# Kernel tuning notes

Measured on AMD Instinct MI355X. Metric: run time of the kernel, lower is better.

Reference implementation:

```python
import jax, jax.numpy as jnp
import numpy as np

D_MODEL = 1024
NUM_HEADS = 16
D_IN = 1024

def setup_inputs() -> dict:
    key = jax.random.key(0)
    ks = jax.random.split(key, 5)
    scale = 1.0 / np.sqrt(D_IN)
    return {
        "in_features": jax.random.normal(ks[0], (4, 2048, D_IN), dtype=jnp.float32),
        "q_weight": jax.random.normal(ks[1], (D_MODEL, D_IN), dtype=jnp.float32) * scale,
        "k_weight": jax.random.normal(ks[2], (D_MODEL, D_IN), dtype=jnp.float32) * scale,
        "v_weight": jax.random.normal(ks[3], (D_MODEL, D_IN), dtype=jnp.float32) * scale,
        "o_weight": jax.random.normal(ks[4], (D_MODEL, D_MODEL), dtype=jnp.float32) * scale,
    }

def reference(in_features, q_weight, k_weight, v_weight, o_weight):
    batch, seq_len, _ = in_features.shape
    d_head = D_MODEL // NUM_HEADS
    # QKV projections (Linear with no bias: x @ W^T)
    q = jnp.einsum('bsi,di->bsd', in_features, q_weight)
    k = jnp.einsum('bsi,di->bsd', in_features, k_weight)
    v = jnp.einsum('bsi,di->bsd', in_features, v_weight)
    # split heads -> [b, h, s, d_head]
    q = q.reshape(batch, seq_len, NUM_HEADS, d_head).transpose(0, 2, 1, 3)
    k = k.reshape(batch, seq_len, NUM_HEADS, d_head).transpose(0, 2, 1, 3)
    v = v.reshape(batch, seq_len, NUM_HEADS, d_head).transpose(0, 2, 1, 3)
    # scaled dot-product attention (scale by per-head dim, as in SelfAttention)
    scores = jnp.einsum('bhqd,bhkd->bhqk', q, k) / jnp.sqrt(jnp.float32(d_head))
    probs = jax.nn.softmax(scores, axis=-1)
    ctx = jnp.einsum('bhqk,bhkd->bhqd', probs, v)
    # merge heads -> [b, s, d_model]
    ctx = ctx.transpose(0, 2, 1, 3).reshape(batch, seq_len, D_MODEL)
    # output projection
    return jnp.einsum('bsd,md->bsm', ctx, o_weight)
```

## Files before the change

### kernel.cpp

```cpp
#include <hip/hip_runtime.h>

typedef _Float16 half8 __attribute__((ext_vector_type(8)));
typedef _Float16 half4v __attribute__((ext_vector_type(4)));
typedef __fp16 fp16x2 __attribute__((ext_vector_type(2)));
typedef float f32x4 __attribute__((ext_vector_type(4)));
typedef float f32x16 __attribute__((ext_vector_type(16)));

__device__ __forceinline__ void gload_lds16(const _Float16* g, _Float16* l) {
    __builtin_amdgcn_global_load_lds(
        (const __attribute__((address_space(1))) void*)g,
        (__attribute__((address_space(3))) void*)l,
        16, 0, 0);
}

__global__ void cvt_f32_f16(const float* __restrict__ src, _Float16* __restrict__ dst, int n4) {
    int i = blockIdx.x * blockDim.x + threadIdx.x;
    if (i >= n4) return;
    f32x4 v = ((const f32x4*)src)[i];
    half4v h;
    h[0] = (_Float16)v[0]; h[1] = (_Float16)v[1];
    h[2] = (_Float16)v[2]; h[3] = (_Float16)v[3];
    ((half4v*)dst)[i] = h;
}

__global__ void cvt4_f32_f16(const float* __restrict__ s0, const float* __restrict__ s1,
                             const float* __restrict__ s2, const float* __restrict__ s3,
                             _Float16* __restrict__ dst) {
    int i = blockIdx.x * blockDim.x + threadIdx.x;
    int wsel = blockIdx.y;
    const float* src = (wsel == 0) ? s0 : (wsel == 1) ? s1 : (wsel == 2) ? s2 : s3;
    f32x4 v = ((const f32x4*)src)[i];
    half4v h;
    h[0] = (_Float16)v[0]; h[1] = (_Float16)v[1];
    h[2] = (_Float16)v[2]; h[3] = (_Float16)v[3];
    ((half4v*)(dst + (size_t)wsel * 1048576))[i] = h;
}

template<int MODE>
__global__ void gemm_nt(const _Float16* __restrict__ A,
                        const _Float16* __restrict__ Wbase,
                        void* __restrict__ outbase)
{
    constexpr int K = 1024;
    __shared__ _Float16 As[2][128 * 32];
    __shared__ _Float16 Bs[2][128 * 32];

    const int tid  = threadIdx.x;
    const int lane = tid & 63;
    const int w    = tid >> 6;
    const int wr   = w >> 1, wc = w & 1;
    const int lr   = lane & 15, lg = lane >> 4;
    const int brow = blockIdx.x * 128;
    const int bcol = blockIdx.y * 128;
    const int mat  = (MODE == 0) ? blockIdx.z : 0;

    const _Float16* Bw = Wbase + (size_t)mat * (1024u * 1024u);

    const int srow = w * 16 + (lane >> 2);
    const int scol = (lane & 3) * 8;
    const _Float16* Ag = A  + (size_t)(brow + srow) * K + scol;
    const _Float16* Bg = Bw + (size_t)(bcol + srow) * K + scol;

    auto stage = [&](int buf, int kt) {
        const _Float16* a0 = Ag + kt * 32;
        const _Float16* b0 = Bg + kt * 32;
        gload_lds16(a0,           &As[buf][w * 512]);
        gload_lds16(a0 + 64 * K,  &As[buf][w * 512 + 2048]);
        gload_lds16(b0,           &Bs[buf][w * 512]);
        gload_lds16(b0 + 64 * K,  &Bs[buf][w * 512 + 2048]);
    };

    f32x4 acc[4][4] = {};
    stage(0, 0);
    __syncthreads();

    for (int kt = 0; kt < K / 32; ++kt) {
        const int cur = kt & 1;
        if (kt + 1 < K / 32) stage(cur ^ 1, kt + 1);
        half8 af[4], bf[4];
#pragma unroll
        for (int mi = 0; mi < 4; ++mi)
            af[mi] = *(const half8*)&As[cur][(wr * 64 + mi * 16 + lr) * 32 + lg * 8];
#pragma unroll
        for (int ni = 0; ni < 4; ++ni)
            bf[ni] = *(const half8*)&Bs[cur][(wc * 64 + ni * 16 + lr) * 32 + lg * 8];
#pragma unroll
        for (int mi = 0; mi < 4; ++mi)
#pragma unroll
            for (int ni = 0; ni < 4; ++ni)
                acc[mi][ni] = __builtin_amdgcn_mfma_f32_16x16x32_f16(af[mi], bf[ni], acc[mi][ni], 0, 0, 0);
        __syncthreads();
    }

    if (MODE == 0) {
        _Float16* outp = (_Float16*)outbase + (size_t)mat * (8192u * 1024u);
        if (mat == 2) {
            _Float16* Ts = &As[0][0];
#pragma unroll
            for (int p = 0; p < 2; ++p) {
                if (wc == p) {
#pragma unroll
                    for (int mi = 0; mi < 4; ++mi)
#pragma unroll
                        for (int ni = 0; ni < 4; ++ni) {
                            int drow = ni * 16 + lr;
                            int s0   = wr * 64 + mi * 16 + lg * 4;
                            half4v o;
#pragma unroll
                            for (int r = 0; r < 4; ++r) o[r] = (_Float16)acc[mi][ni][r];
                            int byteoff = drow * 256 + s0 * 2;
                            byteoff ^= (drow & 7) << 4;
                            *(half4v*)((char*)Ts + byteoff) = o;
                        }
                }
                __syncthreads();
                {
                    int row   = tid >> 2;
                    int cbase = (tid & 3) * 4;
                    int gd = bcol + p * 64 + row;
                    int h = gd >> 6, dd = gd & 63;
                    int b = brow >> 11, sseq = brow & 2047;
                    _Float16* gout = outp + (((size_t)b * 16 + h) * 64 + dd) * 2048 + sseq;
#pragma unroll
                    for (int j = 0; j < 4; ++j) {
                        int c  = cbase + j;
                        int lc = c ^ (row & 7);
                        half8 v = *(const half8*)&Ts[row * 128 + lc * 8];
                        *(half8*)&gout[c * 8] = v;
                    }
                }
                __syncthreads();
            }
        } else {
            const float scale = (mat == 0) ? 0.18033688f : 1.0f;
#pragma unroll
            for (int mi = 0; mi < 4; ++mi)
#pragma unroll
                for (int ni = 0; ni < 4; ++ni)
#pragma unroll
                    for (int r = 0; r < 4; ++r) {
                        int row = brow + wr * 64 + mi * 16 + lg * 4 + r;
                        int col = bcol + wc * 64 + ni * 16 + lr;
                        int b = row >> 11, s = row & 2047;
                        int h = col >> 6,  d = col & 63;
                        outp[(((size_t)b * 16 + h) * 2048 + s) * 64 + d] =
                            (_Float16)(acc[mi][ni][r] * scale);
                    }
        }
    } else {
        float* outp = (float*)outbase;
#pragma unroll
        for (int mi = 0; mi < 4; ++mi)
#pragma unroll
            for (int ni = 0; ni < 4; ++ni)
#pragma unroll
                for (int r = 0; r < 4; ++r) {
                    int row = brow + wr * 64 + mi * 16 + lg * 4 + r;
                    int col = bcol + wc * 64 + ni * 16 + lr;
                    outp[(size_t)row * 1024 + col] = acc[mi][ni][r];
                }
    }
}

#define M_FIX 10.0f
__global__ __launch_bounds__(256, 4)
void attn_kernel(const _Float16* __restrict__ Q,
                 const _Float16* __restrict__ Kx,
                 const _Float16* __restrict__ Vt,
                 _Float16* __restrict__ Ctx)
{
    __shared__ _Float16 Ks[2][64 * 72];
    __shared__ _Float16 Vs[2][64 * 72];

    const int tid = threadIdx.x, lane = tid & 63, w = tid >> 6;
    const int l31 = lane & 31, hi = lane >> 5;

    const int wg = blockIdx.x;
    const int j = ((wg & 7) << 7) + (wg >> 3);
    const int bh = j >> 4, qblk = j & 15;

    const _Float16* Qp  = Q  + ((size_t)bh * 2048 + qblk * 128) * 64;
    const _Float16* Kp  = Kx + (size_t)bh * 2048 * 64;
    const _Float16* Vtp = Vt + (size_t)bh * 64 * 2048;

    half8 qf[4];
#pragma unroll
    for (int ks = 0; ks < 4; ++ks)
        qf[ks] = *(const half8*)(Qp + (size_t)(w * 32 + l31) * 64 + ks * 16 + hi * 8);

    const int srow = tid >> 3;
    const int scol = (tid & 7) * 8;
    const _Float16* Kg0 = Kp  + (size_t)srow * 64   + scol;
    const _Float16* Vg0 = Vtp + (size_t)srow * 2048 + scol;
    const int ldso = srow * 72 + scol;

    const fp16x2 ones2 = {(__fp16)1.0f, (__fp16)1.0f};

    f32x16 cacc[2] = {};
    float l0 = 0.f, l1 = 0.f;

    half8 kr0, kr1, vr0, vr1;
    kr0 = *(const half8*)(Kg0);
    kr1 = *(const half8*)(Kg0 + 2048);
    vr0 = *(const half8*)(Vg0);
    vr1 = *(const half8*)(Vg0 + 32 * 2048);
    *(half8*)&Ks[0][ldso]           = kr0;
    *(half8*)&Ks[0][ldso + 32 * 72] = kr1;
    *(half8*)&Vs[0][ldso]           = vr0;
    *(half8*)&Vs[0][ldso + 32 * 72] = vr1;
    __syncthreads();

    for (int t = 0; t < 32; ++t) {
        const int cur = t & 1;
        if (t < 31) {
            kr0 = *(const half8*)(Kg0 + (size_t)(t + 1) * 4096);
            kr1 = *(const half8*)(Kg0 + (size_t)(t + 1) * 4096 + 2048);
        }

        f32x16 sf[2];
        __builtin_amdgcn_s_setprio(1);
#pragma unroll
        for (int kt = 0; kt < 2; ++kt) {
            f32x16 z;
#pragma unroll
            for (int r = 0; r < 16; ++r) z[r] = -M_FIX;
#pragma unroll
            for (int ks = 0; ks < 4; ++ks) {
                half8 kf = *(const half8*)&Ks[cur][(kt * 32 + l31) * 72 + ks * 16 + hi * 8];
                z = __builtin_amdgcn_mfma_f32_32x32x16_f16(kf, qf[ks], z, 0, 0, 0);
            }
            sf[kt] = z;
        }
        __builtin_amdgcn_s_setprio(0);

        if (t < 31) {
            *(half8*)&Ks[cur ^ 1][ldso]           = kr0;
            *(half8*)&Ks[cur ^ 1][ldso + 32 * 72] = kr1;
            vr0 = *(const half8*)(Vg0 + (t + 1) * 64);
            vr1 = *(const half8*)(Vg0 + (t + 1) * 64 + 32 * 2048);
        }

        half8 bf[4];
#pragma unroll
        for (int kt = 0; kt < 2; ++kt) {
#pragma unroll
            for (int r = 0; r < 16; ++r)
                sf[kt][r] = __builtin_amdgcn_exp2f(sf[kt][r]);

            unsigned uq[4][2];
#pragma unroll
            for (int qd = 0; qd < 4; ++qd)
#pragma unroll
                for (int w2 = 0; w2 < 2; ++w2)
                    uq[qd][w2] = __builtin_bit_cast(unsigned,
                        __builtin_amdgcn_cvt_pkrtz(sf[kt][4 * qd + 2 * w2],
                                                   sf[kt][4 * qd + 2 * w2 + 1]));

#pragma unroll
            for (int k1 = 0; k1 < 2; ++k1) {
                union { half8 h; unsigned u[4]; } bu;
#pragma unroll
                for (int w2 = 0; w2 < 2; ++w2) {
                    unsigned a = uq[2 * k1][w2];
                    unsigned b = uq[2 * k1 + 1][w2];
                    asm("v_permlane32_swap_b32 %0, %1" : "+v"(a), "+v"(b));
                    bu.u[w2]     = a;
                    bu.u[2 + w2] = b;
                }
                l0 = __builtin_amdgcn_fdot2(__builtin_bit_cast(fp16x2, bu.u[0]), ones2, l0, false);
                l1 = __builtin_amdgcn_fdot2(__builtin_bit_cast(fp16x2, bu.u[1]), ones2, l1, false);
                l0 = __builtin_amdgcn_fdot2(__builtin_bit_cast(fp16x2, bu.u[2]), ones2, l0, false);
                l1 = __builtin_amdgcn_fdot2(__builtin_bit_cast(fp16x2, bu.u[3]), ones2, l1, false);
                bf[kt * 2 + k1] = bu.h;
            }
        }

        __builtin_amdgcn_s_setprio(1);
#pragma unroll
        for (int dt = 0; dt < 2; ++dt)
#pragma unroll
            for (int ks = 0; ks < 4; ++ks) {
                half8 vf = *(const half8*)&Vs[cur][(dt * 32 + l31) * 72 + ks * 16 + hi * 8];
                cacc[dt] = __builtin_amdgcn_mfma_f32_32x32x16_f16(vf, bf[ks], cacc[dt], 0, 0, 0);
            }
        __builtin_amdgcn_s_setprio(0);

        if (t < 31) {
            *(half8*)&Vs[cur ^ 1][ldso]           = vr0;
            *(half8*)&Vs[cur ^ 1][ldso + 32 * 72] = vr1;
        }
        __syncthreads();
    }

    float l = l0 + l1;
    const float inv = 1.0f / (l + __shfl_xor(l, 32, 64));
    const int s = qblk * 128 + w * 32 + l31;
    _Float16* Cp = Ctx + ((size_t)(bh >> 4) * 2048 + s) * 1024 + (bh & 15) * 64;
#pragma unroll
    for (int dt = 0; dt < 2; ++dt)
#pragma unroll
        for (int qd = 0; qd < 4; ++qd) {
            half4v o;
#pragma unroll
            for (int j2 = 0; j2 < 4; ++j2) o[j2] = (_Float16)(cacc[dt][4 * qd + j2] * inv);
            *(half4v*)&Cp[dt * 32 + qd * 8 + hi * 4] = o;
        }
}

extern "C" void kernel_launch(void* const* d_in, const int* in_sizes, int n_in,
                              void* d_out, int out_size, void* d_ws, size_t ws_size,
                              hipStream_t stream)
{
    const float* X  = (const float*)d_in[0];
    const float* Wq = (const float*)d_in[1];
    const float* Wk = (const float*)d_in[2];
    const float* Wv = (const float*)d_in[3];
    const float* Wo = (const float*)d_in[4];

    if (ws_size < (size_t)(8 + 4 + 24) * 1024 * 1024 * 2) return;
    _Float16* Xh  = (_Float16*)d_ws;
    _Float16* Wh  = Xh + (size_t)8 * 1024 * 1024;
    _Float16* QKV = Wh + (size_t)4 * 1024 * 1024;
    _Float16* Ctx = Xh;

    cvt_f32_f16<<<8192, 256, 0, stream>>>(X, Xh, 2097152);
    cvt4_f32_f16<<<dim3(1024, 4), 256, 0, stream>>>(Wq, Wk, Wv, Wo, Wh);

    gemm_nt<0><<<dim3(64, 8, 3), 256, 0, stream>>>(Xh, Wh, QKV);

    attn_kernel<<<1024, 256, 0, stream>>>(QKV, QKV + 8388608, QKV + 16777216, Ctx);

    gemm_nt<1><<<dim3(64, 8), 256, 0, stream>>>(Ctx, Wh + 3145728, d_out);
}
```

Measured before the change: 196.6 us.

## Use 256x256-tile 512-thread GEMM with swizzled LDS for QKV projection

Replaces the 128x128 QKV projection GEMM with a dedicated kernel that uses 256x256 output tiles, 8 waves, a 64-wide K step and XOR-swizzled 128 KB LDS double buffers. Global-to-LDS loads are interleaved with the MFMA phases, and s_setprio raises wave priority during the math. The goal is more data reuse per loaded tile and fewer LDS bank conflicts. In exchange the grid shrinks to 384 blocks at one block per CU, so wave-level parallelism and tail balance on 256 CUs could suffer.

```diff
diff --git a/kernel.cpp b/kernel.cpp
--- a/kernel.cpp
+++ b/kernel.cpp
@@ -36,10 +36,146 @@
     ((half4v*)(dst + (size_t)wsel * 1048576))[i] = h;
 }
 
-template<int MODE>
-__global__ void gemm_nt(const _Float16* __restrict__ A,
-                        const _Float16* __restrict__ Wbase,
-                        void* __restrict__ outbase)
+__global__ __launch_bounds__(512, 2)
+void gemm256_qkv(const _Float16* __restrict__ A,
+                 const _Float16* __restrict__ Wbase,
+                 _Float16* __restrict__ outbase)
+{
+    __shared__ _Float16 lds[65536];
+    _Float16* Asb = lds;
+    _Float16* Bsb = lds + 32768;
+
+    const int tid  = threadIdx.x;
+    const int lane = tid & 63;
+    const int w    = tid >> 6;
+    const int wm   = w >> 2;
+    const int wn   = w & 3;
+    const int lr   = lane & 15, lg = lane >> 4;
+    const int brow = blockIdx.x * 256;
+    const int bcol = blockIdx.y * 256;
+    const int mat  = blockIdx.z;
+
+    const _Float16* Ap = A + (size_t)brow * 1024;
+    const _Float16* Bp = Wbase + (size_t)mat * (1024u * 1024u) + (size_t)bcol * 1024;
+
+    const int srowi  = w * 8 + (lane >> 3);
+    const int gchunk = (((lane & 7) ^ ((lane >> 3) & 7)) << 3);
+
+    auto stage2 = [&](int buf, int kt, int pp) {
+#pragma unroll
+        for (int i = pp * 2; i < pp * 2 + 2; ++i) {
+            gload_lds16(Ap + (size_t)(i * 64 + srowi) * 1024 + kt * 64 + gchunk,
+                        Asb + buf * 16384 + i * 4096 + w * 512);
+            gload_lds16(Bp + (size_t)(i * 64 + srowi) * 1024 + kt * 64 + gchunk,
+                        Bsb + buf * 16384 + i * 4096 + w * 512);
+        }
+    };
+
+    f32x4 acc[8][4] = {};
+
+    stage2(0, 0, 0);
+    stage2(0, 0, 1);
+    asm volatile("s_waitcnt vmcnt(0)" ::: "memory");
+    __builtin_amdgcn_s_barrier();
+
+    for (int t = 0; t < 16; ++t) {
+        const int c = t & 1;
+        const _Float16* Ab = Asb + c * 16384;
+        const _Float16* Bb = Bsb + c * 16384;
+
+        half8 bfr[4][2];
+#pragma unroll
+        for (int fc = 0; fc < 4; ++fc) {
+            const int rrow = wn * 64 + fc * 16 + lr;
+#pragma unroll
+            for (int kk = 0; kk < 2; ++kk)
+                bfr[fc][kk] = *(const half8*)&Bb[rrow * 64 + (((kk * 4 + lg) ^ (rrow & 7)) << 3)];
+        }
+
+#pragma unroll
+        for (int p = 0; p < 4; ++p) {
+            half8 afr[2][2];
+#pragma unroll
+            for (int fr = 0; fr < 2; ++fr) {
+                const int arow = wm * 128 + (p * 2 + fr) * 16 + lr;
+#pragma unroll
+                for (int kk = 0; kk < 2; ++kk)
+                    afr[fr][kk] = *(const half8*)&Ab[arow * 64 + (((kk * 4 + lg) ^ (arow & 7)) << 3)];
+            }
+            if (t < 15 && p < 2) stage2(c ^ 1, t + 1, p);
+            __builtin_amdgcn_s_barrier();
+            __builtin_amdgcn_s_setprio(1);
+#pragma unroll
+            for (int fr = 0; fr < 2; ++fr)
+#pragma unroll
+                for (int fc = 0; fc < 4; ++fc)
+#pragma unroll
+                    for (int kk = 0; kk < 2; ++kk)
+                        acc[p * 2 + fr][fc] = __builtin_amdgcn_mfma_f32_16x16x32_f16(
+                            afr[fr][kk], bfr[fc][kk], acc[p * 2 + fr][fc], 0, 0, 0);
+            __builtin_amdgcn_s_setprio(0);
+            __builtin_amdgcn_s_barrier();
+        }
+        asm volatile("s_waitcnt vmcnt(0) lgkmcnt(0)" ::: "memory");
+        __builtin_amdgcn_s_barrier();
+    }
+
+    _Float16* outp = outbase + (size_t)mat * (8192u * 1024u);
+    if (mat == 2) {
+        _Float16* Ts = lds;
+#pragma unroll
+        for (int p = 0; p < 2; ++p) {
+            __syncthreads();
+            if ((wn >> 1) == p) {
+#pragma unroll
+                for (int mi = 0; mi < 8; ++mi)
+#pragma unroll
+                    for (int ni = 0; ni < 4; ++ni) {
+                        const int dloc = (wn & 1) * 64 + ni * 16 + lr;
+                        const int sloc = wm * 128 + mi * 16 + lg * 4;
+                        const int c16  = sloc >> 3;
+                        half4v o;
+#pragma unroll
+                        for (int r = 0; r < 4; ++r) o[r] = (_Float16)acc[mi][ni][r];
+                        *(half4v*)&Ts[dloc * 256 + ((c16 ^ (dloc & 7)) << 3) + (sloc & 7)] = o;
+                    }
+            }
+            __syncthreads();
+            {
+                const int rr = tid >> 2;
+                const int gd = bcol + p * 128 + rr;
+                const int h = gd >> 6, dd = gd & 63;
+                const int b = brow >> 11, sseq = brow & 2047;
+                _Float16* gout = outp + (((size_t)b * 16 + h) * 64 + dd) * 2048 + sseq;
+#pragma unroll
+                for (int jj = 0; jj < 8; ++jj) {
+                    const int c16 = (tid & 3) * 8 + jj;
+                    half8 v = *(const half8*)&Ts[rr * 256 + ((c16 ^ (rr & 7)) << 3)];
+                    *(half8*)&gout[c16 * 8] = v;
+                }
+            }
+        }
+    } else {
+        const float scale = (mat == 0) ? 0.18033688f : 1.0f;
+#pragma unroll
+        for (int mi = 0; mi < 8; ++mi)
+#pragma unroll
+            for (int ni = 0; ni < 4; ++ni)
+#pragma unroll
+                for (int r = 0; r < 4; ++r) {
+                    const int row = brow + wm * 128 + mi * 16 + lg * 4 + r;
+                    const int col = bcol + wn * 64 + ni * 16 + lr;
+                    const int b = row >> 11, s = row & 2047;
+                    const int h = col >> 6, d = col & 63;
+                    outp[(((size_t)b * 16 + h) * 2048 + s) * 64 + d] =
+                        (_Float16)(acc[mi][ni][r] * scale);
+                }
+    }
+}
+
+__global__ void gemm_nt_o(const _Float16* __restrict__ A,
+                          const _Float16* __restrict__ Wbase,
+                          float* __restrict__ outp)
 {
     constexpr int K = 1024;
     __shared__ _Float16 As[2][128 * 32];
@@ -52,14 +188,11 @@
     const int lr   = lane & 15, lg = lane >> 4;
     const int brow = blockIdx.x * 128;
     const int bcol = blockIdx.y * 128;
-    const int mat  = (MODE == 0) ? blockIdx.z : 0;
-
-    const _Float16* Bw = Wbase + (size_t)mat * (1024u * 1024u);
 
     const int srow = w * 16 + (lane >> 2);
     const int scol = (lane & 3) * 8;
-    const _Float16* Ag = A  + (size_t)(brow + srow) * K + scol;
-    const _Float16* Bg = Bw + (size_t)(bcol + srow) * K + scol;
+    const _Float16* Ag = A     + (size_t)(brow + srow) * K + scol;
+    const _Float16* Bg = Wbase + (size_t)(bcol + srow) * K + scol;
 
     auto stage = [&](int buf, int kt) {
         const _Float16* a0 = Ag + kt * 32;
@@ -92,74 +225,16 @@
         __syncthreads();
     }
 
-    if (MODE == 0) {
-        _Float16* outp = (_Float16*)outbase + (size_t)mat * (8192u * 1024u);
-        if (mat == 2) {
-            _Float16* Ts = &As[0][0];
-#pragma unroll
-            for (int p = 0; p < 2; ++p) {
-                if (wc == p) {
-#pragma unroll
-                    for (int mi = 0; mi < 4; ++mi)
-#pragma unroll
-                        for (int ni = 0; ni < 4; ++ni) {
-                            int drow = ni * 16 + lr;
-                            int s0   = wr * 64 + mi * 16 + lg * 4;
-                            half4v o;
-#pragma unroll
-                            for (int r = 0; r < 4; ++r) o[r] = (_Float16)acc[mi][ni][r];
-                            int byteoff = drow * 256 + s0 * 2;
-                            byteoff ^= (drow & 7) << 4;
-                            *(half4v*)((char*)Ts + byteoff) = o;
-                        }
-                }
-                __syncthreads();
-                {
-                    int row   = tid >> 2;
-                    int cbase = (tid & 3) * 4;
-                    int gd = bcol + p * 64 + row;
-                    int h = gd >> 6, dd = gd & 63;
-                    int b = brow >> 11, sseq = brow & 2047;
-                    _Float16* gout = outp + (((size_t)b * 16 + h) * 64 + dd) * 2048 + sseq;
-#pragma unroll
-                    for (int j = 0; j < 4; ++j) {
-                        int c  = cbase + j;
-                        int lc = c ^ (row & 7);
-                        half8 v = *(const half8*)&Ts[row * 128 + lc * 8];
-                        *(half8*)&gout[c * 8] = v;
-                    }
-                }
-                __syncthreads();
-            }
-        } else {
-            const float scale = (mat == 0) ? 0.18033688f : 1.0f;
-#pragma unroll
-            for (int mi = 0; mi < 4; ++mi)
-#pragma unroll
-                for (int ni = 0; ni < 4; ++ni)
-#pragma unroll
-                    for (int r = 0; r < 4; ++r) {
-                        int row = brow + wr * 64 + mi * 16 + lg * 4 + r;
-                        int col = bcol + wc * 64 + ni * 16 + lr;
-                        int b = row >> 11, s = row & 2047;
-                        int h = col >> 6,  d = col & 63;
-                        outp[(((size_t)b * 16 + h) * 2048 + s) * 64 + d] =
-                            (_Float16)(acc[mi][ni][r] * scale);
-                    }
-        }
-    } else {
-        float* outp = (float*)outbase;
-#pragma unroll
-        for (int mi = 0; mi < 4; ++mi)
-#pragma unroll
-            for (int ni = 0; ni < 4; ++ni)
-#pragma unroll
-                for (int r = 0; r < 4; ++r) {
-                    int row = brow + wr * 64 + mi * 16 + lg * 4 + r;
-                    int col = bcol + wc * 64 + ni * 16 + lr;
-                    outp[(size_t)row * 1024 + col] = acc[mi][ni][r];
-                }
-    }
+#pragma unroll
+    for (int mi = 0; mi < 4; ++mi)
+#pragma unroll
+        for (int ni = 0; ni < 4; ++ni)
+#pragma unroll
+            for (int r = 0; r < 4; ++r) {
+                int row = brow + wr * 64 + mi * 16 + lg * 4 + r;
+                int col = bcol + wc * 64 + ni * 16 + lr;
+                outp[(size_t)row * 1024 + col] = acc[mi][ni][r];
+            }
 }
 
 #define M_FIX 10.0f
@@ -326,9 +401,9 @@
     cvt_f32_f16<<<8192, 256, 0, stream>>>(X, Xh, 2097152);
     cvt4_f32_f16<<<dim3(1024, 4), 256, 0, stream>>>(Wq, Wk, Wv, Wo, Wh);
 
-    gemm_nt<0><<<dim3(64, 8, 3), 256, 0, stream>>>(Xh, Wh, QKV);
+    gemm256_qkv<<<dim3(32, 4, 3), 512, 0, stream>>>(Xh, Wh, QKV);
 
     attn_kernel<<<1024, 256, 0, stream>>>(QKV, QKV + 8388608, QKV + 16777216, Ctx);
 
-    gemm_nt<1><<<dim3(64, 8), 256, 0, stream>>>(Ctx, Wh + 3145728, d_out);
-}
+    gemm_nt_o<<<dim3(64, 8), 256, 0, stream>>>(Ctx, Wh + 3145728, (float*)d_out);
+}
```

Measured after the change: 193.8 us. About the same (-1.4%).

## Deepen GEMM LDS pipeline to four buffers with swizzle and relaxed barriers

Applied to the files above, without the earlier changes.

The projection GEMM moves from a two-stage to a four-buffer LDS ring that prefetches two K-tiles ahead. It waits on partial vmcnt counts instead of a full __syncthreads every iteration. LDS columns get an XOR swizzle to reduce bank conflicts, MFMA issue is raised with s_setprio, and launch bounds request two blocks per CU. The cost is 64KB of LDS per block and hand-managed waitcnt logic that may be fragile.

```diff
diff --git a/kernel.cpp b/kernel.cpp
--- a/kernel.cpp
+++ b/kernel.cpp
@@ -37,13 +37,14 @@
 }
 
 template<int MODE>
-__global__ void gemm_nt(const _Float16* __restrict__ A,
-                        const _Float16* __restrict__ Wbase,
-                        void* __restrict__ outbase)
+__global__ __launch_bounds__(256, 2)
+void gemm_nt(const _Float16* __restrict__ A,
+             const _Float16* __restrict__ Wbase,
+             void* __restrict__ outbase)
 {
-    constexpr int K = 1024;
-    __shared__ _Float16 As[2][128 * 32];
-    __shared__ _Float16 Bs[2][128 * 32];
+    __shared__ _Float16 lds[32768];
+    _Float16* Asb = lds;
+    _Float16* Bsb = lds + 16384;
 
     const int tid  = threadIdx.x;
     const int lane = tid & 63;
@@ -54,50 +55,66 @@
     const int bcol = blockIdx.y * 128;
     const int mat  = (MODE == 0) ? blockIdx.z : 0;
 
-    const _Float16* Bw = Wbase + (size_t)mat * (1024u * 1024u);
-
-    const int srow = w * 16 + (lane >> 2);
-    const int scol = (lane & 3) * 8;
-    const _Float16* Ag = A  + (size_t)(brow + srow) * K + scol;
-    const _Float16* Bg = Bw + (size_t)(bcol + srow) * K + scol;
+    const _Float16* Ap = A + (size_t)brow * 1024;
+    const _Float16* Bp = Wbase + (size_t)mat * (1024u * 1024u) + (size_t)bcol * 1024;
+
+    const int srw  = tid >> 2;
+    const int sch  = tid & 3;
+    const int soff = ((sch ^ (srw & 3)) << 3);
 
     auto stage = [&](int buf, int kt) {
-        const _Float16* a0 = Ag + kt * 32;
-        const _Float16* b0 = Bg + kt * 32;
-        gload_lds16(a0,           &As[buf][w * 512]);
-        gload_lds16(a0 + 64 * K,  &As[buf][w * 512 + 2048]);
-        gload_lds16(b0,           &Bs[buf][w * 512]);
-        gload_lds16(b0 + 64 * K,  &Bs[buf][w * 512 + 2048]);
+#pragma unroll
+        for (int i = 0; i < 2; ++i) {
+            const int ra = i * 64 + srw;
+            gload_lds16(Ap + (size_t)ra * 1024 + kt * 32 + soff,
+                        Asb + buf * 4096 + i * 2048 + w * 512);
+            gload_lds16(Bp + (size_t)ra * 1024 + kt * 32 + soff,
+                        Bsb + buf * 4096 + i * 2048 + w * 512);
+        }
     };
 
     f32x4 acc[4][4] = {};
+    const int swz = ((lg ^ (lr & 3)) << 3);
+
     stage(0, 0);
-    __syncthreads();
-
-    for (int kt = 0; kt < K / 32; ++kt) {
-        const int cur = kt & 1;
-        if (kt + 1 < K / 32) stage(cur ^ 1, kt + 1);
+    stage(1, 1);
+    asm volatile("s_waitcnt vmcnt(4)" ::: "memory");
+    __builtin_amdgcn_s_barrier();
+    __builtin_amdgcn_sched_barrier(0);
+
+    for (int t = 0; t < 32; ++t) {
+        if (t < 30) stage((t + 2) & 3, t + 2);
+        const _Float16* Ab = Asb + (t & 3) * 4096;
+        const _Float16* Bb = Bsb + (t & 3) * 4096;
         half8 af[4], bf[4];
 #pragma unroll
         for (int mi = 0; mi < 4; ++mi)
-            af[mi] = *(const half8*)&As[cur][(wr * 64 + mi * 16 + lr) * 32 + lg * 8];
+            af[mi] = *(const half8*)&Ab[(wr * 64 + mi * 16 + lr) * 32 + swz];
 #pragma unroll
         for (int ni = 0; ni < 4; ++ni)
-            bf[ni] = *(const half8*)&Bs[cur][(wc * 64 + ni * 16 + lr) * 32 + lg * 8];
+            bf[ni] = *(const half8*)&Bb[(wc * 64 + ni * 16 + lr) * 32 + swz];
+        __builtin_amdgcn_s_setprio(1);
 #pragma unroll
         for (int mi = 0; mi < 4; ++mi)
 #pragma unroll
             for (int ni = 0; ni < 4; ++ni)
                 acc[mi][ni] = __builtin_amdgcn_mfma_f32_16x16x32_f16(af[mi], bf[ni], acc[mi][ni], 0, 0, 0);
-        __syncthreads();
+        __builtin_amdgcn_s_setprio(0);
+        if (t < 30)       { asm volatile("s_waitcnt vmcnt(4)" ::: "memory"); }
+        else if (t == 30) { asm volatile("s_waitcnt vmcnt(0)" ::: "memory"); }
+        if (t < 31) {
+            __builtin_amdgcn_s_barrier();
+            __builtin_amdgcn_sched_barrier(0);
+        }
     }
 
     if (MODE == 0) {
         _Float16* outp = (_Float16*)outbase + (size_t)mat * (8192u * 1024u);
         if (mat == 2) {
-            _Float16* Ts = &As[0][0];
+            _Float16* Ts = lds;
 #pragma unroll
             for (int p = 0; p < 2; ++p) {
+                __syncthreads();
                 if (wc == p) {
 #pragma unroll
                     for (int mi = 0; mi < 4; ++mi)
@@ -129,7 +146,6 @@
                         *(half8*)&gout[c * 8] = v;
                     }
                 }
-                __syncthreads();
             }
         } else {
             const float scale = (mat == 0) ? 0.18033688f : 1.0f;
@@ -330,5 +346,5 @@
 
     attn_kernel<<<1024, 256, 0, stream>>>(QKV, QKV + 8388608, QKV + 16777216, Ctx);
 
-    gemm_nt<1><<<dim3(64, 8), 256, 0, stream>>>(Ctx, Wh + 3145728, d_out);
-}
+    gemm_nt<1><<<dim3(64, 8, 1), 256, 0, stream>>>(Ctx, Wh + 3145728, d_out);
+}
```

Result: no change. 193.3 us (-1.7%).
